# Performance work log

Hardware: AMD Instinct MI355X
Metric: run time of the kernel (lower is better)

Reference implementation:

```python
import jax, jax.numpy as jnp
import numpy as np

N_NODES = 50000
N_EDGES = 600000
D_IN = 128
D_OUT = 128
N_BASES = 4
N_RATINGS = 5


def setup_inputs() -> dict:
    key = jax.random.key(0)
    k1, k2, k3, k4, k5, k6 = jax.random.split(key, 6)
    x = jax.random.normal(k1, (N_NODES, D_IN), dtype=jnp.float32)
    edge_index = jax.random.randint(k2, (2, N_EDGES), 0, N_NODES, dtype=jnp.int64)
    edge_type = jax.random.randint(k3, (N_EDGES,), 0, N_RATINGS, dtype=jnp.int64)
    # basis matrices B_k: (out, in); a_r stacked over ratings: (R, K); W_0: (out, in)
    B = jax.random.normal(k4, (N_BASES, D_OUT, D_IN), dtype=jnp.float32) * 0.05
    A = jax.random.normal(k5, (N_RATINGS, N_BASES), dtype=jnp.float32) * 0.05
    W0 = jax.random.normal(k6, (D_OUT, D_IN), dtype=jnp.float32) * 0.05
    return {"x": x, "edge_index": edge_index, "edge_type": edge_type, "B": B, "A": A, "W0": W0}


def reference(x, edge_index, edge_type, B, A, W0):
    # self-loop term: (W0 @ x^T)^T == x @ W0^T
    n_nodes = x.shape[0]
    src, tgt = edge_index[0], edge_index[1]
    out = x @ W0.T  # [N, out]
    # per-relation basis-composed weights W_r = sum_k a_r[k] * B_k  -> [R, out, in]
    W = jnp.einsum('rk,kod->rod', A, B)
    n_ratings = A.shape[0]
    for r in range(n_ratings):  # small fixed relation set
        h = x @ W[r].T                     # [N, out] transform once per node
        msg = jnp.where((edge_type == r)[:, None], h[src], jnp.float32(0))  # [E, out]
        out = out + jax.ops.segment_sum(msg, tgt, num_segments=n_nodes)
    return out
```

## Files before the change

### kernel.cpp

```cpp
#include <hip/hip_runtime.h>

#define N_NODES 50000
#define N_EDGES 600000
#define D 128
#define NB_SCAN 196

typedef __attribute__((ext_vector_type(8))) short short8;
typedef __attribute__((ext_vector_type(4))) float float4v;

static __device__ __forceinline__ float bf2f(unsigned int u16) {
    union { unsigned int i; float f; } v; v.i = u16 << 16; return v.f;
}
static __device__ __forceinline__ unsigned short f2bf(float f) {
    union { float f; unsigned int i; } v; v.f = f;
    unsigned int u = v.i;
    return (unsigned short)((u + 0x7FFFu + ((u >> 16) & 1u)) >> 16);
}
static __device__ __forceinline__ float h2f(unsigned int h) {
    unsigned int s = (h >> 15) & 1u, e = (h >> 10) & 0x1fu, m = h & 0x3ffu;
    unsigned int bits = (e == 0) ? (s << 31)
                                 : ((s << 31) | ((e + 112u) << 23) | (m << 13));
    union { unsigned int i; float f; } v; v.i = bits; return v.f;
}

__global__ __launch_bounds__(256) void setup(int* __restrict__ flags,
                                             int* __restrict__ cnt,
                                             unsigned int* __restrict__ scanst) {
    int i = blockIdx.x * 256 + threadIdx.x;
    if (i < N_NODES) cnt[i] = 0;
    if (i < 8) flags[i] = 0;
    if (i < 200) scanst[i] = 0;
}

__global__ __launch_bounds__(256) void detect_all(const int* __restrict__ ei,
                                                  const int* __restrict__ et,
                                                  const unsigned int* __restrict__ x,
                                                  const unsigned int* __restrict__ B,
                                                  const unsigned int* __restrict__ A,
                                                  const unsigned int* __restrict__ W0,
                                                  int* __restrict__ flags) {
    __shared__ int sflag;
    if (threadIdx.x == 0) sflag = 0;
    __syncthreads();
    int b = blockIdx.x, acc = 0, fidx;
    if (b < 192) {
        fidx = 0;
        for (int i = b * 256 + threadIdx.x; i < N_EDGES; i += 192 * 256)
            acc |= ei[2 * i + 1];
    } else if (b < 240) {
        fidx = 1;
        for (int i = (b - 192) * 256 + threadIdx.x; i < N_EDGES / 2; i += 48 * 256)
            acc |= et[2 * i + 1];
    } else if (b < 288) {
        fidx = 2;
        for (int i = (b - 240) * 256 + threadIdx.x; i < 600000; i += 48 * 256) {
            unsigned int e = (x[i] >> 7) & 0xffu;
            acc |= (e > 0xA0u || e < 0x50u) ? 1 : 0;
        }
    } else if (b < 300) {
        fidx = 3;
        for (int i = (b - 288) * 256 + threadIdx.x; i < 32768; i += 12 * 256) {
            unsigned int e = (B[i] >> 7) & 0xffu;
            acc |= (e > 0xA0u || e < 0x50u) ? 1 : 0;
        }
    } else if (b == 300) {
        fidx = 4;
        for (int i = threadIdx.x; i < 10; i += 256) {
            unsigned int e = (A[i] >> 7) & 0xffu;
            acc |= (e > 0xA0u || e < 0x50u) ? 1 : 0;
        }
    } else if (b < 307) {
        fidx = 5;
        for (int i = (b - 301) * 256 + threadIdx.x; i < 8192; i += 6 * 256) {
            unsigned int e = (W0[i] >> 7) & 0xffu;
            acc |= (e > 0xA0u || e < 0x50u) ? 1 : 0;
        }
    } else {
        fidx = 6;
        for (int i = (b - 307) * 256 + threadIdx.x; i < 300000; i += 48 * 256) {
            unsigned int el = (x[i] >> 7) & 0xffu, eh = (x[i] >> 23) & 0xffu;
            acc |= (el < 0x58u || eh < 0x58u) ? 1 : 0;
        }
    }
    if (acc) sflag = 1;
    __syncthreads();
    if (threadIdx.x == 0 && sflag) atomicOr(flags + fidx, 1);
}

static __device__ __forceinline__ float loadw(const void* p, int idx, int f32) {
    return f32 ? ((const float*)p)[idx] : bf2f(((const unsigned short*)p)[idx]);
}

__global__ __launch_bounds__(256) void norm_hist_w(const int* __restrict__ ei,
                                                   const int* __restrict__ et,
                                                   int* __restrict__ idx32,
                                                   int* __restrict__ et32,
                                                   int* __restrict__ cnt,
                                                   const void* __restrict__ A,
                                                   const void* __restrict__ B,
                                                   const void* __restrict__ W0,
                                                   unsigned short* __restrict__ wcatW,
                                                   const int* __restrict__ flags) {
    int b = blockIdx.x;
    if (b < 4688) {
        int i = b * 256 + threadIdx.x;
        if (i < 2 * N_EDGES) {
            int v = flags[0] ? ei[i] : ei[2 * i];
            idx32[i] = v;
            if (i >= N_EDGES && (unsigned)v < (unsigned)N_NODES)
                atomicAdd(&cnt[v], 1);
        }
    } else if (b < 7032) {
        int i = (b - 4688) * 256 + threadIdx.x;
        if (i < N_EDGES) et32[i] = flags[1] ? et[i] : et[2 * i];
    } else {
        int idx = (b - 7032) * 256 + threadIdx.x;
        int fB = flags[3], fA = flags[4], fW = flags[5];
        int f = idx >> 7, d = idx & 127;
        int slot = f >> 7, o = f & 127;
        float v;
        if (slot == 0) {
            v = loadw(W0, o * D + d, fW);
        } else {
            int r = slot - 1;
            v = 0.f;
#pragma unroll
            for (int j = 0; j < 4; ++j)
                v += loadw(A, r * 4 + j, fA) * loadw(B, (j * D + o) * D + d, fB);
        }
        wcatW[idx] = f2bf(v);
    }
}

__global__ __launch_bounds__(256) void prep_wt6_direct(const void* __restrict__ A,
                                                       const void* __restrict__ B,
                                                       const void* __restrict__ W0,
                                                       float* __restrict__ wcatT6F,
                                                       const int* __restrict__ flags) {
    int idx = blockIdx.x * 256 + threadIdx.x;
    int fB = flags[3], fA = flags[4], fW = flags[5];
    int slot = idx >> 14, d = (idx >> 7) & 127, o = idx & 127;
    float v;
    if (slot == 0) {
        v = loadw(W0, o * D + d, fW);
    } else {
        int r = slot - 1;
        v = 0.f;
#pragma unroll
        for (int j = 0; j < 4; ++j)
            v += loadw(A, r * 4 + j, fA) * loadw(B, (j * D + o) * D + d, fB);
    }
    wcatT6F[idx] = v;
}

#define SWZ(row, cb) ((row) * 256 + ((cb) ^ (((row) & 7) << 4)))
__global__ __launch_bounds__(256) void gemm_y(const void* __restrict__ xraw,
                                              const unsigned short* __restrict__ wcatW,
                                              unsigned short* __restrict__ Ybf,
                                              const int* __restrict__ flags) {
    __shared__ __align__(16) char lds[49152];
    char* xsb = lds;
    char* wsb = lds + 16384;
    int tid = threadIdx.x;
    int m0 = blockIdx.x * 64;
    int wid = tid >> 6, lane = tid & 63;
    int wf = (wid & 1) * 64;
    int wn2 = (wid >> 1) * 32;
    int lm = lane & 15, kg = lane >> 4;
    int f32 = flags[2], f16 = flags[6];
    const short8 z8 = {0, 0, 0, 0, 0, 0, 0, 0};

    {
        int row = tid >> 2, cb0 = (tid & 3) * 64;
        int gm = m0 + row;
#pragma unroll
        for (int q = 0; q < 4; ++q) {
            int cb = cb0 + q * 16;
            short8 av;
            if (gm >= N_NODES) {
                av = z8;
            } else if (f32) {
                const float4* xp = (const float4*)xraw + (((size_t)gm * D) >> 2) + (cb >> 4) * 2;
                float4 u0 = xp[0], u1 = xp[1];
                union { short8 s; unsigned short h[8]; } pk;
                pk.h[0] = f2bf(u0.x); pk.h[1] = f2bf(u0.y);
                pk.h[2] = f2bf(u0.z); pk.h[3] = f2bf(u0.w);
                pk.h[4] = f2bf(u1.x); pk.h[5] = f2bf(u1.y);
                pk.h[6] = f2bf(u1.z); pk.h[7] = f2bf(u1.w);
                av = pk.s;
            } else if (f16) {
                const uint4* xp4 = (const uint4*)xraw + (((size_t)gm * D) >> 3) + (cb >> 4);
                uint4 u = *xp4;
                unsigned int ww[4] = {u.x, u.y, u.z, u.w};
                union { short8 s; unsigned short h[8]; } pk;
#pragma unroll
                for (int z = 0; z < 4; ++z) {
                    pk.h[2 * z]     = f2bf(h2f(ww[z] & 0xffffu));
                    pk.h[2 * z + 1] = f2bf(h2f(ww[z] >> 16));
                }
                av = pk.s;
            } else {
                const uint4* xp4 = (const uint4*)xraw + (((size_t)gm * D) >> 3) + (cb >> 4);
                union { uint4 v; short8 s; } cv; cv.v = *xp4;
                av = cv.s;
            }
            *(short8*)(xsb + SWZ(row, cb)) = av;
        }
    }

    short8 wr[8];
    {
        int row = tid >> 1, c0h = (tid & 1) * 64;
        const unsigned short* wp = wcatW + (size_t)row * D + c0h;
#pragma unroll
        for (int q = 0; q < 8; ++q) wr[q] = *(const short8*)(wp + q * 8);
    }

    for (int nt = 0; nt < 6; ++nt) {
        if (nt) __syncthreads();
        {
            int row = tid >> 1, cb0 = (tid & 1) * 128;
#pragma unroll
            for (int q = 0; q < 8; ++q)
                *(short8*)(wsb + SWZ(row, cb0 + q * 16)) = wr[q];
        }
        if (nt + 1 < 6) {
            int row = tid >> 1, c0h = (tid & 1) * 64;
            const unsigned short* wp = wcatW + (size_t)((nt + 1) * 128 + row) * D + c0h;
#pragma unroll
            for (int q = 0; q < 8; ++q) wr[q] = *(const short8*)(wp + q * 8);
        }
        __syncthreads();

        float4v accf[4][2];
#pragma unroll
        for (int i = 0; i < 4; ++i)
#pragma unroll
            for (int j = 0; j < 2; ++j) accf[i][j] = (float4v){0.f, 0.f, 0.f, 0.f};

#pragma unroll
        for (int kb = 0; kb < 4; ++kb) {
            int kcb = kb * 64 + kg * 16;
            short8 a[4], b[2];
#pragma unroll
            for (int i = 0; i < 4; ++i)
                a[i] = *(const short8*)(wsb + SWZ(wf + i * 16 + lm, kcb));
#pragma unroll
            for (int j = 0; j < 2; ++j)
                b[j] = *(const short8*)(xsb + SWZ(wn2 + j * 16 + lm, kcb));
#pragma unroll
            for (int i = 0; i < 4; ++i)
#pragma unroll
                for (int j = 0; j < 2; ++j)
                    accf[i][j] = __builtin_amdgcn_mfma_f32_16x16x32_bf16(a[i], b[j], accf[i][j], 0, 0, 0);
        }

#pragma unroll
        for (int i = 0; i < 4; ++i) {
            int f0 = nt * 128 + wf + i * 16 + kg * 4;
#pragma unroll
            for (int j = 0; j < 2; ++j) {
                int node = m0 + wn2 + j * 16 + lm;
                if (node < N_NODES) {
                    union { unsigned long long u; unsigned short h[4]; } pk;
                    pk.h[0] = f2bf(accf[i][j][0]); pk.h[1] = f2bf(accf[i][j][1]);
                    pk.h[2] = f2bf(accf[i][j][2]); pk.h[3] = f2bf(accf[i][j][3]);
                    *(unsigned long long*)(Ybf + (size_t)node * 768 + f0) = pk.u;
                }
            }
        }
    }
}

#define SC_AGG (1u << 30)
#define SC_PRE (1u << 31)
__global__ __launch_bounds__(256) void scan_place(const int* __restrict__ cnt,
                                                  int* __restrict__ offsets,
                                                  int* __restrict__ cursor,
                                                  unsigned int* __restrict__ scanst,
                                                  const int* __restrict__ src,
                                                  const int* __restrict__ tgt,
                                                  const int* __restrict__ et,
                                                  int* __restrict__ entries) {
    __shared__ int sh[256];
    __shared__ int sbid, sprefix;
    unsigned int* status = scanst;
    unsigned int* ticket = scanst + 196;
    unsigned int* done   = scanst + 197;
    int t = threadIdx.x;
    if (t == 0) sbid = (int)atomicAdd(ticket, 1u);
    __syncthreads();
    int bid = sbid;
    int idx = bid * 256 + t;
    int v = (idx < N_NODES) ? cnt[idx] : 0;
    sh[t] = v;
    __syncthreads();
    for (int off = 1; off < 256; off <<= 1) {
        int a = (t >= off) ? sh[t - off] : 0;
        __syncthreads();
        sh[t] += a;
        __syncthreads();
    }
    if (t == 0) {
        int total = sh[255];
        atomicExch(&status[bid], (unsigned int)total | SC_AGG);
        int prefix = 0;
        for (int j = bid - 1; j >= 0; --j) {
            unsigned int s;
            do { s = atomicAdd(&status[j], 0u); } while ((s & (SC_AGG | SC_PRE)) == 0u);
            prefix += (int)(s & 0x3FFFFFFFu);
            if (s & SC_PRE) break;
        }
        atomicExch(&status[bid], (unsigned int)(prefix + total) | SC_PRE);
        sprefix = prefix;
    }
    __syncthreads();
    int excl = sh[t] - v + sprefix;
    if (idx < N_NODES) {
        offsets[idx] = excl;
        atomicExch(&cursor[idx], excl);
        if (idx == N_NODES - 1) offsets[N_NODES] = excl + v;
    }
    __syncthreads();
    if (t == 0) {
        atomicAdd(done, 1u);
        while (atomicAdd(done, 0u) < (unsigned)NB_SCAN) __builtin_amdgcn_s_sleep(1);
    }
    __syncthreads();
    int e0 = bid * 3062;
    int e1 = e0 + 3062; if (e1 > N_EDGES) e1 = N_EDGES;
    for (int e = e0 + t; e < e1; e += 256) {
        int s = src[e], g = tgt[e], r = et[e];
        if ((unsigned)s >= (unsigned)N_NODES || (unsigned)g >= (unsigned)N_NODES || (unsigned)r >= 5u) continue;
        int pos = atomicAdd(&cursor[g], 1);
        entries[pos] = s * 8 + r;
    }
}

__global__ __launch_bounds__(256) void agg_out(const int* __restrict__ offsets,
                                               const int* __restrict__ entries,
                                               const unsigned int* __restrict__ Y32,
                                               float* __restrict__ outF) {
    int tid = threadIdx.x;
    int wid = tid >> 6, lane = tid & 63;
    int n = __builtin_amdgcn_readfirstlane(blockIdx.x * 4 + wid);
    int beg = __builtin_amdgcn_readfirstlane(offsets[n]);
    int end = __builtin_amdgcn_readfirstlane(offsets[n + 1]);
    unsigned int selfw = Y32[(size_t)n * 384 + lane];
    float a0 = bf2f(selfw & 0xffffu), a1 = bf2f(selfw >> 16);

    for (int base = beg; base < end; base += 64) {
        int cnt = end - base;
        if (cnt > 64) cnt = 64;
        int eload = entries[base + lane];
        int j = 0;
        for (; j + 3 < cnt; j += 4) {
            int en0 = __builtin_amdgcn_readlane(eload, j);
            int en1 = __builtin_amdgcn_readlane(eload, j + 1);
            int en2 = __builtin_amdgcn_readlane(eload, j + 2);
            int en3 = __builtin_amdgcn_readlane(eload, j + 3);
            unsigned int r0 = (unsigned)(en0 >> 3) < (unsigned)N_NODES ? (unsigned)(en0 >> 3) : 0u;
            unsigned int r1 = (unsigned)(en1 >> 3) < (unsigned)N_NODES ? (unsigned)(en1 >> 3) : 0u;
            unsigned int r2 = (unsigned)(en2 >> 3) < (unsigned)N_NODES ? (unsigned)(en2 >> 3) : 0u;
            unsigned int r3 = (unsigned)(en3 >> 3) < (unsigned)N_NODES ? (unsigned)(en3 >> 3) : 0u;
            unsigned int x0 = Y32[(size_t)r0 * 384 + ((en0 & 7) + 1) * 64 + lane];
            unsigned int x1 = Y32[(size_t)r1 * 384 + ((en1 & 7) + 1) * 64 + lane];
            unsigned int x2 = Y32[(size_t)r2 * 384 + ((en2 & 7) + 1) * 64 + lane];
            unsigned int x3 = Y32[(size_t)r3 * 384 + ((en3 & 7) + 1) * 64 + lane];
            a0 += bf2f(x0 & 0xffffu); a1 += bf2f(x0 >> 16);
            a0 += bf2f(x1 & 0xffffu); a1 += bf2f(x1 >> 16);
            a0 += bf2f(x2 & 0xffffu); a1 += bf2f(x2 >> 16);
            a0 += bf2f(x3 & 0xffffu); a1 += bf2f(x3 >> 16);
        }
        for (; j < cnt; ++j) {
            int en = __builtin_amdgcn_readlane(eload, j);
            unsigned int rr = (unsigned)(en >> 3) < (unsigned)N_NODES ? (unsigned)(en >> 3) : 0u;
            unsigned int xw = Y32[(size_t)rr * 384 + ((en & 7) + 1) * 64 + lane];
            a0 += bf2f(xw & 0xffffu); a1 += bf2f(xw >> 16);
        }
    }

    *((float2*)outF + (size_t)n * 64 + lane) = make_float2(a0, a1);
}

static __device__ __forceinline__ float2 readx2(const void* x, int node, int lane,
                                                int f32, int f16) {
    if (f32) return *((const float2*)x + (size_t)node * 64 + lane);
    unsigned int w = *((const unsigned int*)x + (size_t)node * 64 + lane);
    float2 r;
    if (f16) { r.x = h2f(w & 0xffffu); r.y = h2f(w >> 16); }
    else     { r.x = bf2f(w & 0xffffu); r.y = bf2f(w >> 16); }
    return r;
}

__global__ __launch_bounds__(256) void self_raw(const void* __restrict__ x,
                                                const float* __restrict__ wcatT6F,
                                                float* __restrict__ outF,
                                                const int* __restrict__ flags) {
    int t = blockIdx.x * 256 + threadIdx.x;
    int n = t >> 6, lane = t & 63;
    int f32 = flags[2], f16 = flags[6];
    float2 xp = readx2(x, n, lane, f32, f16);
    float m0 = 0.f, m1 = 0.f;
#pragma unroll 8
    for (int dp = 0; dp < 64; ++dp) {
        float xa = __shfl(xp.x, dp);
        float xc = __shfl(xp.y, dp);
        float2 w0 = *(const float2*)(wcatT6F + (size_t)(2 * dp) * D + 2 * lane);
        float2 w1 = *(const float2*)(wcatT6F + (size_t)(2 * dp + 1) * D + 2 * lane);
        m0 += xa * w0.x + xc * w1.x;
        m1 += xa * w0.y + xc * w1.y;
    }
    *((float2*)outF + (size_t)n * 64 + lane) = make_float2(m0, m1);
}

__global__ __launch_bounds__(256) void edge_raw(const int* __restrict__ src,
                                                const int* __restrict__ tgt,
                                                const int* __restrict__ et,
                                                const void* __restrict__ x,
                                                const float* __restrict__ wcatT6F,
                                                float* __restrict__ outF,
                                                const int* __restrict__ flags) {
    int t = blockIdx.x * 256 + threadIdx.x;
    int e = t >> 6, lane = t & 63;
    if (e >= N_EDGES) return;
    int f32 = flags[2], f16 = flags[6];
    int s = src[e], g = tgt[e], r = et[e];
    if ((unsigned)s >= (unsigned)N_NODES || (unsigned)g >= (unsigned)N_NODES || (unsigned)r >= 5u) return;
    float2 xp = readx2(x, s, lane, f32, f16);
    const float* wt = wcatT6F + (size_t)(1 + r) * D * D;
    float m0 = 0.f, m1 = 0.f;
#pragma unroll 8
    for (int dp = 0; dp < 64; ++dp) {
        float xa = __shfl(xp.x, dp);
        float xc = __shfl(xp.y, dp);
        float2 w0 = *(const float2*)(wt + (size_t)(2 * dp) * D + 2 * lane);
        float2 w1 = *(const float2*)(wt + (size_t)(2 * dp + 1) * D + 2 * lane);
        m0 += xa * w0.x + xc * w1.x;
        m1 += xa * w0.y + xc * w1.y;
    }
    float* ap = outF + (size_t)g * D + lane * 2;
    atomicAdd(ap + 0, m0);
    atomicAdd(ap + 1, m1);
}

extern "C" void kernel_launch(void* const* d_in, const int* in_sizes, int n_in,
                              void* d_out, int out_size, void* d_ws, size_t ws_size,
                              hipStream_t stream) {
    const void* x  = nullptr; const int* ei = nullptr; const int* et = nullptr;
    const void* B  = nullptr; const void* A = nullptr; const void* W0 = nullptr;
    for (int i = 0; i < n_in; ++i) {
        switch (in_sizes[i]) {
            case 6400000: x  = d_in[i]; break;
            case 1200000: ei = (const int*)d_in[i]; break;
            case 600000:  et = (const int*)d_in[i]; break;
            case 65536:   B  = d_in[i]; break;
            case 20:      A  = d_in[i]; break;
            case 16384:   W0 = d_in[i]; break;
            default: break;
        }
    }
    if (!x || !ei || !et || !B || !A || !W0) {
        x  = d_in[0]; ei = (const int*)d_in[1]; et = (const int*)d_in[2];
        B  = d_in[3]; A  = d_in[4]; W0 = d_in[5];
    }
    float* outF = (float*)d_out;

    char* ws = (char*)d_ws;
    int*   flags   = (int*)(ws + 0);
    float* wcatT6F = (float*)(ws + 256);
    unsigned short* wcatW = (unsigned short*)(ws + 393472);
    int* offsets  = (int*)(ws + 590080);
    int* cursor   = (int*)(ws + 790144);
    int* cnt      = (int*)(ws + 990144);
    unsigned int* scanst = (unsigned int*)(ws + 1190144);
    int* entries  = (int*)(ws + 1191168);
    int* idx32    = (int*)(ws + 3591168);
    int* et32     = (int*)(ws + 8391168);
    unsigned short* Y = (unsigned short*)(ws + 10791168);
    const size_t needMain = 10791168ull + 76800000ull;
    const size_t needT3   = 393472ull;

    int* src32 = idx32;
    int* tgt32 = idx32 + N_EDGES;

    setup<<<NB_SCAN, 256, 0, stream>>>(flags, cnt, scanst);
    detect_all<<<355, 256, 0, stream>>>(ei, et, (const unsigned int*)x,
                                        (const unsigned int*)B, (const unsigned int*)A,
                                        (const unsigned int*)W0, flags);

    if (ws_size >= needMain) {
        norm_hist_w<<<7416, 256, 0, stream>>>(ei, et, idx32, et32, cnt,
                                              A, B, W0, wcatW, flags);
        gemm_y<<<782, 256, 0, stream>>>(x, wcatW, Y, flags);
        scan_place<<<NB_SCAN, 256, 0, stream>>>(cnt, offsets, cursor, scanst,
                                                src32, tgt32, et32, entries);
        agg_out<<<12500, 256, 0, stream>>>(offsets, entries, (const unsigned int*)Y, outF);
    } else if (ws_size >= needT3) {
        prep_wt6_direct<<<384, 256, 0, stream>>>(A, B, W0, wcatT6F, flags);
        self_raw<<<12500, 256, 0, stream>>>(x, wcatT6F, outF, flags);
        edge_raw<<<150000, 256, 0, stream>>>(ei, ei + N_EDGES, et, x, wcatT6F, outF, flags);
    }
}
```

Measured before the change: 245.0 us.

## Drop LDS staging in gemm_y, load MFMA operands directly into registers

The node-feature GEMM no longer stages x and weight tiles through shared memory with barriers. Each wave loads its x fragments once into registers and reads weight fragments straight from global memory (cache-resident) for every output tile. Blocks shrink to 128 threads covering 32 nodes, doubling the grid. This removes LDS traffic and syncs, at the cost of redundant global/L2 weight reads and less reuse per block.

```diff
diff --git a/kernel.cpp b/kernel.cpp
--- a/kernel.cpp
+++ b/kernel.cpp
@@ -153,44 +153,43 @@
     wcatT6F[idx] = v;
 }
 
-#define SWZ(row, cb) ((row) * 256 + ((cb) ^ (((row) & 7) << 4)))
-__global__ __launch_bounds__(256) void gemm_y(const void* __restrict__ xraw,
+__global__ __launch_bounds__(128) void gemm_y(const void* __restrict__ xraw,
                                               const unsigned short* __restrict__ wcatW,
                                               unsigned short* __restrict__ Ybf,
                                               const int* __restrict__ flags) {
-    __shared__ __align__(16) char lds[49152];
-    char* xsb = lds;
-    char* wsb = lds + 16384;
     int tid = threadIdx.x;
-    int m0 = blockIdx.x * 64;
+    int m0 = blockIdx.x * 32;
     int wid = tid >> 6, lane = tid & 63;
-    int wf = (wid & 1) * 64;
-    int wn2 = (wid >> 1) * 32;
+    int wf = wid * 64;
     int lm = lane & 15, kg = lane >> 4;
     int f32 = flags[2], f16 = flags[6];
     const short8 z8 = {0, 0, 0, 0, 0, 0, 0, 0};
 
-    {
-        int row = tid >> 2, cb0 = (tid & 3) * 64;
-        int gm = m0 + row;
-#pragma unroll
-        for (int q = 0; q < 4; ++q) {
-            int cb = cb0 + q * 16;
-            short8 av;
-            if (gm >= N_NODES) {
-                av = z8;
-            } else if (f32) {
-                const float4* xp = (const float4*)xraw + (((size_t)gm * D) >> 2) + (cb >> 4) * 2;
-                float4 u0 = xp[0], u1 = xp[1];
+    short8 xb[2][4];
+#pragma unroll
+    for (int j = 0; j < 2; ++j) {
+        int node = m0 + j * 16 + lm;
+        if (node >= N_NODES) {
+#pragma unroll
+            for (int kb = 0; kb < 4; ++kb) xb[j][kb] = z8;
+        } else if (f32) {
+            const float4* xp = (const float4*)xraw + (((size_t)node * D) >> 2);
+#pragma unroll
+            for (int kb = 0; kb < 4; ++kb) {
+                float4 u0 = xp[kb * 8 + kg * 2];
+                float4 u1 = xp[kb * 8 + kg * 2 + 1];
                 union { short8 s; unsigned short h[8]; } pk;
                 pk.h[0] = f2bf(u0.x); pk.h[1] = f2bf(u0.y);
                 pk.h[2] = f2bf(u0.z); pk.h[3] = f2bf(u0.w);
                 pk.h[4] = f2bf(u1.x); pk.h[5] = f2bf(u1.y);
                 pk.h[6] = f2bf(u1.z); pk.h[7] = f2bf(u1.w);
-                av = pk.s;
-            } else if (f16) {
-                const uint4* xp4 = (const uint4*)xraw + (((size_t)gm * D) >> 3) + (cb >> 4);
-                uint4 u = *xp4;
+                xb[j][kb] = pk.s;
+            }
+        } else if (f16) {
+            const uint4* xp4 = (const uint4*)xraw + (((size_t)node * D) >> 3);
+#pragma unroll
+            for (int kb = 0; kb < 4; ++kb) {
+                uint4 u = xp4[kb * 4 + kg];
                 unsigned int ww[4] = {u.x, u.y, u.z, u.w};
                 union { short8 s; unsigned short h[8]; } pk;
 #pragma unroll
@@ -198,61 +197,40 @@
                     pk.h[2 * z]     = f2bf(h2f(ww[z] & 0xffffu));
                     pk.h[2 * z + 1] = f2bf(h2f(ww[z] >> 16));
                 }
-                av = pk.s;
-            } else {
-                const uint4* xp4 = (const uint4*)xraw + (((size_t)gm * D) >> 3) + (cb >> 4);
-                union { uint4 v; short8 s; } cv; cv.v = *xp4;
-                av = cv.s;
+                xb[j][kb] = pk.s;
             }
-            *(short8*)(xsb + SWZ(row, cb)) = av;
-        }
-    }
-
-    short8 wr[8];
-    {
-        int row = tid >> 1, c0h = (tid & 1) * 64;
-        const unsigned short* wp = wcatW + (size_t)row * D + c0h;
-#pragma unroll
-        for (int q = 0; q < 8; ++q) wr[q] = *(const short8*)(wp + q * 8);
+        } else {
+            const uint4* xp4 = (const uint4*)xraw + (((size_t)node * D) >> 3);
+#pragma unroll
+            for (int kb = 0; kb < 4; ++kb) {
+                union { uint4 v; short8 s; } cv; cv.v = xp4[kb * 4 + kg];
+                xb[j][kb] = cv.s;
+            }
+        }
     }
 
     for (int nt = 0; nt < 6; ++nt) {
-        if (nt) __syncthreads();
-        {
-            int row = tid >> 1, cb0 = (tid & 1) * 128;
-#pragma unroll
-            for (int q = 0; q < 8; ++q)
-                *(short8*)(wsb + SWZ(row, cb0 + q * 16)) = wr[q];
-        }
-        if (nt + 1 < 6) {
-            int row = tid >> 1, c0h = (tid & 1) * 64;
-            const unsigned short* wp = wcatW + (size_t)((nt + 1) * 128 + row) * D + c0h;
-#pragma unroll
-            for (int q = 0; q < 8; ++q) wr[q] = *(const short8*)(wp + q * 8);
-        }
-        __syncthreads();
-
-        float4v accf[4][2];
+        const unsigned short* wp = wcatW + (size_t)(nt * 128 + wf + lm) * D + kg * 8;
+        float4v acc[4][2];
 #pragma unroll
         for (int i = 0; i < 4; ++i)
 #pragma unroll
-            for (int j = 0; j < 2; ++j) accf[i][j] = (float4v){0.f, 0.f, 0.f, 0.f};
+            for (int j = 0; j < 2; ++j) acc[i][j] = (float4v){0.f, 0.f, 0.f, 0.f};
 
 #pragma unroll
         for (int kb = 0; kb < 4; ++kb) {
-            int kcb = kb * 64 + kg * 16;
-            short8 a[4], b[2];
-#pragma unroll
-            for (int i = 0; i < 4; ++i)
-                a[i] = *(const short8*)(wsb + SWZ(wf + i * 16 + lm, kcb));
-#pragma unroll
-            for (int j = 0; j < 2; ++j)
-                b[j] = *(const short8*)(xsb + SWZ(wn2 + j * 16 + lm, kcb));
-#pragma unroll
-            for (int i = 0; i < 4; ++i)
-#pragma unroll
-                for (int j = 0; j < 2; ++j)
-                    accf[i][j] = __builtin_amdgcn_mfma_f32_16x16x32_bf16(a[i], b[j], accf[i][j], 0, 0, 0);
+            short8 a0 = *(const short8*)(wp + kb * 32 + 0 * 16 * D);
+            short8 a1 = *(const short8*)(wp + kb * 32 + 1 * 16 * D);
+            short8 a2 = *(const short8*)(wp + kb * 32 + 2 * 16 * D);
+            short8 a3 = *(const short8*)(wp + kb * 32 + 3 * 16 * D);
+            acc[0][0] = __builtin_amdgcn_mfma_f32_16x16x32_bf16(a0, xb[0][kb], acc[0][0], 0, 0, 0);
+            acc[0][1] = __builtin_amdgcn_mfma_f32_16x16x32_bf16(a0, xb[1][kb], acc[0][1], 0, 0, 0);
+            acc[1][0] = __builtin_amdgcn_mfma_f32_16x16x32_bf16(a1, xb[0][kb], acc[1][0], 0, 0, 0);
+            acc[1][1] = __builtin_amdgcn_mfma_f32_16x16x32_bf16(a1, xb[1][kb], acc[1][1], 0, 0, 0);
+            acc[2][0] = __builtin_amdgcn_mfma_f32_16x16x32_bf16(a2, xb[0][kb], acc[2][0], 0, 0, 0);
+            acc[2][1] = __builtin_amdgcn_mfma_f32_16x16x32_bf16(a2, xb[1][kb], acc[2][1], 0, 0, 0);
+            acc[3][0] = __builtin_amdgcn_mfma_f32_16x16x32_bf16(a3, xb[0][kb], acc[3][0], 0, 0, 0);
+            acc[3][1] = __builtin_amdgcn_mfma_f32_16x16x32_bf16(a3, xb[1][kb], acc[3][1], 0, 0, 0);
         }
 
 #pragma unroll
@@ -260,11 +238,11 @@
             int f0 = nt * 128 + wf + i * 16 + kg * 4;
 #pragma unroll
             for (int j = 0; j < 2; ++j) {
-                int node = m0 + wn2 + j * 16 + lm;
+                int node = m0 + j * 16 + lm;
                 if (node < N_NODES) {
                     union { unsigned long long u; unsigned short h[4]; } pk;
-                    pk.h[0] = f2bf(accf[i][j][0]); pk.h[1] = f2bf(accf[i][j][1]);
-                    pk.h[2] = f2bf(accf[i][j][2]); pk.h[3] = f2bf(accf[i][j][3]);
+                    pk.h[0] = f2bf(acc[i][j][0]); pk.h[1] = f2bf(acc[i][j][1]);
+                    pk.h[2] = f2bf(acc[i][j][2]); pk.h[3] = f2bf(acc[i][j][3]);
                     *(unsigned long long*)(Ybf + (size_t)node * 768 + f0) = pk.u;
                 }
             }
@@ -492,7 +470,7 @@
     if (ws_size >= needMain) {
         norm_hist_w<<<7416, 256, 0, stream>>>(ei, et, idx32, et32, cnt,
                                               A, B, W0, wcatW, flags);
-        gemm_y<<<782, 256, 0, stream>>>(x, wcatW, Y, flags);
+        gemm_y<<<1563, 128, 0, stream>>>(x, wcatW, Y, flags);
         scan_place<<<NB_SCAN, 256, 0, stream>>>(cnt, offsets, cursor, scanst,
                                                 src32, tgt32, et32, entries);
         agg_out<<<12500, 256, 0, stream>>>(offsets, entries, (const unsigned int*)Y, outF);
```

Result: slower. 265.4 us (+8.3%).
